# Kernel optimization log

Measured on AMD Instinct MI355X. Metric: run time of the kernel, lower is better.

## Reference

```python
import jax, jax.numpy as jnp
import numpy as np

N = 50000      # nodes
E = 800000     # edges (before self-loops)
H = 4          # heads
C = 64         # hidden channels per head
CLS = 10       # len(bins)+1
D_IN = 64      # input feature dim
NEG_SLOPE = 0.2


def setup_inputs() -> dict:
    key = jax.random.key(0)
    ks = jax.random.split(key, 24)
    inp = {
        "x": jax.random.normal(ks[0], (N, D_IN), jnp.float32),
        "edge_index": jax.random.randint(ks[1], (2, E), 0, N),
    }
    dims = [(D_IN, C), (H * C, C), (H * C, C), (H * C, C), (H * C, CLS)]
    k = 2
    for l, (din, dout) in enumerate(dims):
        sc = 1.0 / np.sqrt(din)
        inp[f"W{l}"] = jax.random.normal(ks[k], (din, H * dout), jnp.float32) * sc; k += 1
        inp[f"as{l}"] = jax.random.normal(ks[k], (H, dout), jnp.float32) * sc; k += 1
        inp[f"ad{l}"] = jax.random.normal(ks[k], (H, dout), jnp.float32) * sc; k += 1
        inp[f"b{l}"] = jnp.zeros((H * dout,), jnp.float32)
    return inp


def gat_layer(x, src, dst, W, a_s, a_d, b):
    # PyG GATConv (concat=True): h = x W -> [N,H,Ch]
    Hh, Ch = a_s.shape
    h = (x @ W).reshape(-1, Hh, Ch)
    asn = (h * a_s).sum(-1)                      # [N,H]
    adn = (h * a_d).sum(-1)                      # [N,H]
    e = jax.nn.leaky_relu(asn[src] + adn[dst], NEG_SLOPE)   # [Et,H]
    m = jax.ops.segment_max(e, dst, num_segments=N)         # softmax over in-edges per dst
    ex = jnp.exp(e - m[dst])
    s = jax.ops.segment_sum(ex, dst, num_segments=N)
    alpha = ex / (s[dst] + 1e-16)                # [Et,H]
    out = jax.ops.segment_sum(alpha[:, :, None] * h[src], dst, num_segments=N)
    return out.reshape(-1, Hh * Ch) + b


def reference(x, edge_index, W0, as0, ad0, b0, W1, as1, ad1, b1,
              W2, as2, ad2, b2, W3, as3, ad3, b3, W4, as4, ad4, b4):
    loop = jnp.arange(N, dtype=edge_index.dtype)  # GATConv add_self_loops=True
    src = jnp.concatenate([edge_index[0], loop])
    dst = jnp.concatenate([edge_index[1], loop])
    params = [(W0, as0, ad0, b0), (W1, as1, ad1, b1), (W2, as2, ad2, b2),
              (W3, as3, ad3, b3), (W4, as4, ad4, b4)]
    for W, a_s, a_d, b in params:
        x = jax.nn.relu(gat_layer(x, src, dst, W, a_s, a_d, b))
        # dropout(p=0.5) is identity in eval mode (training=False)
    return x
```

## Files before the change

kernel.cpp:

```cpp
#include <hip/hip_runtime.h>
#include <hip/hip_bf16.h>
#include <math.h>

#define N_NODES 50000
#define N_PAD   50048
#define N_EDGES 800000
#define HEADS 4

typedef __attribute__((ext_vector_type(8))) _Float16 half8_t;
typedef __attribute__((ext_vector_type(4))) _Float16 half4_t;
typedef __attribute__((ext_vector_type(4))) float f32x4;

__device__ inline void split2(float v, _Float16& p0, _Float16& p1) {
    p0 = (_Float16)v;
    p1 = (_Float16)(v - (float)p0);
}

__device__ inline size_t ktiled_off(int row, int k, size_t rowcap) {
    return (size_t)(k >> 5) * (rowcap * 32) + (size_t)row * 32 +
           ((((k >> 3) & 3) ^ (row & 3)) << 3) + (k & 7);
}


__global__ void init_deg_kernel(int* __restrict__ deg) {
    int i = blockIdx.x * blockDim.x + threadIdx.x;
    if (i < N_NODES) deg[i] = 1;
}

__global__ void hist_kernel(const int* __restrict__ dst, int* __restrict__ deg) {
    int i = blockIdx.x * blockDim.x + threadIdx.x;
    if (i < N_EDGES) atomicAdd(&deg[dst[i]], 1);
}

__global__ __launch_bounds__(1024) void scan_kernel(const int* __restrict__ deg,
                                                    int* __restrict__ rowptr,
                                                    int* __restrict__ cursor) {
    __shared__ int wsums[16];
    const int t = threadIdx.x;
    const int wv = t >> 6, ln = t & 63;
    const int WCHUNK = (N_NODES + 15) / 16;
    const int base = wv * WCHUNK;
    int lim = base + WCHUNK; if (lim > N_NODES) lim = N_NODES;

    int tot = 0;
    for (int i = base + ln; i < lim; i += 64) tot += deg[i];
#pragma unroll
    for (int o = 1; o < 64; o <<= 1) tot += __shfl_xor(tot, o);
    if (ln == 0) wsums[wv] = tot;
    __syncthreads();

    int run = 0;
    for (int w = 0; w < wv; ++w) run += wsums[w];

    for (int i0 = base; i0 < lim; i0 += 64) {
        int i = i0 + ln;
        int d = (i < lim) ? deg[i] : 0;
        int sc = d;
#pragma unroll
        for (int o = 1; o < 64; o <<= 1) {
            int v = __shfl_up(sc, o);
            if (ln >= o) sc += v;
        }
        if (i < lim) {
            int val = run + sc - d;
            rowptr[i] = val;
            cursor[i] = val;
        }
        run += __shfl(sc, 63);
    }
    if (t == 1023) rowptr[N_NODES] = run;
}

__global__ void scatter_kernel(const int* __restrict__ src, const int* __restrict__ dst,
                               int* __restrict__ cursor, int* __restrict__ col) {
    int i = blockIdx.x * blockDim.x + threadIdx.x;
    if (i < N_EDGES) {
        int d = dst[i];
        int pos = atomicAdd(&cursor[d], 1);
        col[pos] = src[i];
    } else if (i < N_EDGES + N_NODES) {
        int n = i - N_EDGES;
        int pos = atomicAdd(&cursor[n], 1);
        col[pos] = n;
    }
}


struct W5 { const float* p[5]; };

__global__ void w_split_kernel(W5 ws, _Float16* __restrict__ wt) {
    int t = blockIdx.x * blockDim.x + threadIdx.x;
    int l = t >> 16;
    int r = t & 65535;
    int c = r >> 8, k = r & 255;
    float v;
    if (l == 0) {
        v = ((k >> 6) == (c >> 6)) ? ws.p[0][(k & 63) * 256 + c] : 0.f;
    } else {
        int K = 256;
        int NC = (l == 4) ? 40 : 256;
        v = (k < K && c < NC) ? ws.p[l][k * NC + c] : 0.f;
    }
    _Float16 a, b;
    split2(v, a, b);
    size_t off = (size_t)l * 131072 + ktiled_off(c, k, 256);
    wt[off] = a;
    wt[65536 + off] = b;
}

__global__ void avec0_kernel(const float* __restrict__ W0,
                             const float* __restrict__ as0, const float* __restrict__ ad0,
                             float* __restrict__ avec, float* __restrict__ dvec) {
    int t = threadIdx.x;
    int hd = t >> 6, k = t & 63;
    float s1 = 0.f, s2 = 0.f;
    for (int c = 0; c < 64; ++c) {
        float w = W0[k * 256 + hd * 64 + c];
        s1 += w * as0[hd * 64 + c];
        s2 += w * ad0[hd * 64 + c];
    }
    avec[t] = s1;
    dvec[t] = s2;
}

__global__ void attn0_kernel(const float* __restrict__ x0,
                             const float* __restrict__ avec, const float* __restrict__ dvec,
                             float* __restrict__ asn, float* __restrict__ adn) {
    int t = blockIdx.x * blockDim.x + threadIdx.x;
    if (t >= N_NODES * HEADS) return;
    int n = t >> 2, hd = t & 3;
    const float* xp = x0 + (size_t)n * 64;
    const float* ap = avec + hd * 64;
    const float* dp = dvec + hd * 64;
    float s1 = 0.f, s2 = 0.f;
    for (int c = 0; c < 64; c += 4) {
        float4 xv = *reinterpret_cast<const float4*>(&xp[c]);
        float4 av = *reinterpret_cast<const float4*>(&ap[c]);
        float4 dv = *reinterpret_cast<const float4*>(&dp[c]);
        s1 += xv.x * av.x + xv.y * av.y + xv.z * av.z + xv.w * av.w;
        s2 += xv.x * dv.x + xv.y * dv.y + xv.z * dv.z + xv.w * dv.w;
    }
    asn[t] = s1;
    adn[t] = s2;
}


__global__ __launch_bounds__(256) void aggregate_x0_kernel(
        const float* __restrict__ x0,
        const float* __restrict__ asn, const float* __restrict__ adn,
        const int* __restrict__ rowptr, const int* __restrict__ col,
        _Float16* __restrict__ pl, size_t pstride) {
    const int n = (blockIdx.x << 2) + (threadIdx.x >> 6);
    const int lane = threadIdx.x & 63;
    const int hdg = lane >> 4;
    const int e16 = lane & 15;

    const int start = rowptr[n];
    const int end = rowptr[n + 1];
    const float adv = adn[(n << 2) | hdg];

    float m = -INFINITY, s = 0.f;
    float a0 = 0.f, a1 = 0.f, a2 = 0.f, a3 = 0.f;

    for (int e0 = start; e0 < end; e0 += 16) {
        int e = e0 + e16;
        int srcl = n;
        float ev = -INFINITY;
        if (e < end) {
            srcl = col[e];
            float t = asn[(srcl << 2) | hdg] + adv;
            ev = (t > 0.f) ? t : 0.2f * t;
        }
        float bm = ev;
#pragma unroll
        for (int o = 1; o < 16; o <<= 1) bm = fmaxf(bm, __shfl_xor(bm, o));
        float mn = fmaxf(m, bm);
        float scale = __expf(m - mn);
        float p = __expf(ev - mn);
        float ps = p;
#pragma unroll
        for (int o = 1; o < 16; o <<= 1) ps += __shfl_xor(ps, o);
        s = s * scale + ps;
        m = mn;

        a0 *= __shfl(scale, 0);
        a1 *= __shfl(scale, 16);
        a2 *= __shfl(scale, 32);
        a3 *= __shfl(scale, 48);

        int cnt = end - e0; if (cnt > 16) cnt = 16;
        int cnt4 = (cnt + 3) & ~3;
        for (int j0 = 0; j0 < cnt4; j0 += 4) {
#pragma unroll
            for (int j = 0; j < 4; ++j) {
                int sj = __shfl(srcl, j0 + j);
                float xv = x0[(size_t)sj * 64 + lane];
                a0 += __shfl(p, j0 + j) * xv;
                a1 += __shfl(p, 16 + j0 + j) * xv;
                a2 += __shfl(p, 32 + j0 + j) * xv;
                a3 += __shfl(p, 48 + j0 + j) * xv;
            }
        }
    }

    float v0 = a0 / (__shfl(s, 0) + 1e-16f);
    float v1 = a1 / (__shfl(s, 16) + 1e-16f);
    float v2 = a2 / (__shfl(s, 32) + 1e-16f);
    float v3 = a3 / (__shfl(s, 48) + 1e-16f);

    float vv[1];
    _Float16 pa, pb;
#define EMIT_Y0(V, HD)                                        \
    {                                                          \
        split2((V), pa, pb);                                   \
        size_t off = ktiled_off(n, (HD) * 64 + lane, N_PAD);   \
        pl[off] = pa;                                          \
        pl[pstride + off] = pb;                                \
    }
    EMIT_Y0(v0, 0) EMIT_Y0(v1, 1) EMIT_Y0(v2, 2) EMIT_Y0(v3, 3)
#undef EMIT_Y0
    (void)vv;
}


template <int FUSE_ATTN>
__global__ __launch_bounds__(256) void gemm_mfma_kernel(
        const _Float16* __restrict__ Apl, size_t apstride,
        const _Float16* __restrict__ Wt,
        float* __restrict__ C, int K, int NC,
        const float* __restrict__ as_flat, const float* __restrict__ ad_flat,
        float* __restrict__ asn, float* __restrict__ adn,
        const float* __restrict__ bias, _Float16* __restrict__ opl, size_t opstride) {
    __shared__ __align__(16) _Float16 lds[2][16384];

    const int tid = threadIdx.x;
    const int lane = tid & 63;
    const int wave = tid >> 6;
    const int wr = (wave >> 1) * 64;
    const int wc = (wave & 1) * 64;
    const int m0 = blockIdx.x * 128;
    const int n0 = blockIdx.y * 128;
    const bool wave_active = (FUSE_ATTN != 2) || ((n0 + wc) < NC);

    f32x4 acc[4][4];
#pragma unroll
    for (int i = 0; i < 4; ++i)
#pragma unroll
        for (int j = 0; j < 4; ++j) acc[i][j] = (f32x4){0.f, 0.f, 0.f, 0.f};

    const _Float16* gptr[8];
    size_t ktstep;
    {
        const _Float16* sbase;
        int rowbase;
        if (wave < 2) {
            sbase = Apl + (size_t)wave * apstride;
            rowbase = m0;
            ktstep = (size_t)N_PAD * 32;
        } else {
            sbase = Wt + (size_t)(wave - 2) * 65536;
            rowbase = n0;
            ktstep = 8192;
        }
#pragma unroll
        for (int it = 0; it < 8; ++it) {
            int idx = it * 64 + lane;
            gptr[it] = sbase + (size_t)(rowbase + (idx >> 2)) * 32 + (idx & 3) * 8;
        }
    }

    const int cswz = ((lane >> 4) ^ (lane & 3)) << 3;
    const int KT = K >> 5;

#pragma unroll
    for (int it = 0; it < 8; ++it) {
        __builtin_amdgcn_global_load_lds(
            (const __attribute__((address_space(1))) void*)gptr[it],
            (__attribute__((address_space(3))) void*)((char*)&lds[0][0] + wave * 8192 + it * 1024),
            16, 0, 0);
    }

    for (int kt = 0; kt < KT; ++kt) {
        __syncthreads();

        if (kt + 1 < KT) {
            char* dstw = (char*)&lds[(kt + 1) & 1][0] + wave * 8192;
#pragma unroll
            for (int it = 0; it < 8; ++it) {
                __builtin_amdgcn_global_load_lds(
                    (const __attribute__((address_space(1))) void*)(gptr[it] + (size_t)(kt + 1) * ktstep),
                    (__attribute__((address_space(3))) void*)(dstw + it * 1024),
                    16, 0, 0);
            }
        }

        if (wave_active) {
            const _Float16* Ab = &lds[kt & 1][0];
            const _Float16* Bb = Ab + 8192;

            half8_t bf[2][4];
#pragma unroll
            for (int p = 0; p < 2; ++p)
#pragma unroll
                for (int j = 0; j < 4; ++j) {
                    int r = wc + j * 16 + (lane & 15);
                    bf[p][j] = *(const half8_t*)(Bb + p * 4096 + r * 32 + cswz);
                }
#pragma unroll
            for (int i = 0; i < 4; ++i) {
                int r = wr + i * 16 + (lane & 15);
                half8_t af0 = *(const half8_t*)(Ab + r * 32 + cswz);
                half8_t af1 = *(const half8_t*)(Ab + 4096 + r * 32 + cswz);
#pragma unroll
                for (int j = 0; j < 4; ++j) {
                    f32x4 c = acc[i][j];
                    c = __builtin_amdgcn_mfma_f32_16x16x32_f16(af0, bf[1][j], c, 0, 0, 0);
                    c = __builtin_amdgcn_mfma_f32_16x16x32_f16(af1, bf[0][j], c, 0, 0, 0);
                    c = __builtin_amdgcn_mfma_f32_16x16x32_f16(af0, bf[0][j], c, 0, 0, 0);
                    acc[i][j] = c;
                }
            }
        }
    }

    const int rbase = m0 + wr + (lane >> 4) * 4;
    const int cbase = n0 + wc + (lane & 15);

    if (FUSE_ATTN == 1) {
#pragma unroll
        for (int i = 0; i < 4; ++i)
#pragma unroll
            for (int j = 0; j < 4; ++j) {
                int gcol = cbase + j * 16;
#pragma unroll
                for (int r4 = 0; r4 < 4; ++r4) {
                    int grow = rbase + i * 16 + r4;
                    if (grow < N_NODES) C[(size_t)grow * 256 + gcol] = acc[i][j][r4];
                }
            }
        const int hd_out = (n0 + wc) >> 6;
        float as_v[4], ad_v[4];
#pragma unroll
        for (int j = 0; j < 4; ++j) {
            int gc = cbase + j * 16;
            as_v[j] = as_flat[gc];
            ad_v[j] = ad_flat[gc];
        }
#pragma unroll
        for (int i = 0; i < 4; ++i)
#pragma unroll
            for (int r4 = 0; r4 < 4; ++r4) {
                float ps = 0.f, pd = 0.f;
#pragma unroll
                for (int j = 0; j < 4; ++j) {
                    float v = acc[i][j][r4];
                    ps += v * as_v[j];
                    pd += v * ad_v[j];
                }
#pragma unroll
                for (int o = 1; o < 16; o <<= 1) {
                    ps += __shfl_xor(ps, o);
                    pd += __shfl_xor(pd, o);
                }
                if ((lane & 15) == 0) {
                    int grow = rbase + i * 16 + r4;
                    if (grow < N_NODES) {
                        asn[grow * 4 + hd_out] = ps;
                        adn[grow * 4 + hd_out] = pd;
                    }
                }
            }
    } else if (FUSE_ATTN == 2) {
#pragma unroll
        for (int i = 0; i < 4; ++i)
#pragma unroll
            for (int j = 0; j < 4; ++j) {
                int gcol = cbase + j * 16;
                if (gcol >= NC) continue;
#pragma unroll
                for (int r4 = 0; r4 < 4; ++r4) {
                    int grow = rbase + i * 16 + r4;
                    if (grow < N_NODES) C[(size_t)grow * NC + gcol] = acc[i][j][r4];
                }
            }
        if (wc == 0) {
            float as_v[4], ad_v[4];
            int hdj[4];
#pragma unroll
            for (int j = 0; j < 4; ++j) {
                int gc = cbase + j * 16;
                bool valj = gc < 40;
                as_v[j] = valj ? as_flat[gc] : 0.f;
                ad_v[j] = valj ? ad_flat[gc] : 0.f;
                hdj[j] = valj ? (gc / 10) : -1;
            }
#pragma unroll
            for (int i = 0; i < 4; ++i)
#pragma unroll
                for (int r4 = 0; r4 < 4; ++r4) {
                    float p0 = 0.f, p1 = 0.f, p2 = 0.f, p3 = 0.f;
                    float q0 = 0.f, q1 = 0.f, q2 = 0.f, q3 = 0.f;
#pragma unroll
                    for (int j = 0; j < 4; ++j) {
                        float v = acc[i][j][r4];
                        float vs = v * as_v[j];
                        float vd = v * ad_v[j];
                        p0 += (hdj[j] == 0) ? vs : 0.f;
                        p1 += (hdj[j] == 1) ? vs : 0.f;
                        p2 += (hdj[j] == 2) ? vs : 0.f;
                        p3 += (hdj[j] == 3) ? vs : 0.f;
                        q0 += (hdj[j] == 0) ? vd : 0.f;
                        q1 += (hdj[j] == 1) ? vd : 0.f;
                        q2 += (hdj[j] == 2) ? vd : 0.f;
                        q3 += (hdj[j] == 3) ? vd : 0.f;
                    }
#pragma unroll
                    for (int o = 1; o < 16; o <<= 1) {
                        p0 += __shfl_xor(p0, o); p1 += __shfl_xor(p1, o);
                        p2 += __shfl_xor(p2, o); p3 += __shfl_xor(p3, o);
                        q0 += __shfl_xor(q0, o); q1 += __shfl_xor(q1, o);
                        q2 += __shfl_xor(q2, o); q3 += __shfl_xor(q3, o);
                    }
                    if ((lane & 15) == 0) {
                        int grow = rbase + i * 16 + r4;
                        if (grow < N_NODES) {
                            asn[grow * 4 + 0] = p0; asn[grow * 4 + 1] = p1;
                            asn[grow * 4 + 2] = p2; asn[grow * 4 + 3] = p3;
                            adn[grow * 4 + 0] = q0; adn[grow * 4 + 1] = q1;
                            adn[grow * 4 + 2] = q2; adn[grow * 4 + 3] = q3;
                        }
                    }
                }
        }
    } else {
#pragma unroll
        for (int i = 0; i < 4; ++i)
#pragma unroll
            for (int j = 0; j < 4; ++j) {
                int gcol = cbase + j * 16;
                float bv = bias[gcol];
#pragma unroll
                for (int r4 = 0; r4 < 4; ++r4) {
                    int grow = rbase + i * 16 + r4;
                    if (grow < N_NODES) {
                        float v = fmaxf(acc[i][j][r4] + bv, 0.f);
                        _Float16 pa, pb;
                        split2(v, pa, pb);
                        size_t off = ktiled_off(grow, gcol, N_PAD);
                        opl[off] = pa;
                        opl[opstride + off] = pb;
                    }
                }
            }
    }
}


__global__ __launch_bounds__(256) void aggregate64_kernel(
        const float* __restrict__ h,
        const float* __restrict__ asn, const float* __restrict__ adn,
        const int* __restrict__ rowptr, const int* __restrict__ col,
        const float* __restrict__ bias,
        _Float16* __restrict__ pl, size_t pstride) {
    const int n = (blockIdx.x << 2) + (threadIdx.x >> 6);
    const int lane = threadIdx.x & 63;
    const int hd = lane >> 4;
    const int e16 = lane & 15;
    const int pbase = lane & 48;

    const int start = rowptr[n];
    const int end = rowptr[n + 1];
    const float adv = adn[(n << 2) | hd];

    float m = -INFINITY, s = 0.f;
    float a0 = 0.f, a1 = 0.f, a2 = 0.f, a3 = 0.f;

    for (int e0 = start; e0 < end; e0 += 16) {
        int e = e0 + e16;
        int srcl = n;
        float ev = -INFINITY;
        if (e < end) {
            srcl = col[e];
            float t = asn[(srcl << 2) | hd] + adv;
            ev = (t > 0.f) ? t : 0.2f * t;
        }
        float bm = ev;
#pragma unroll
        for (int o = 1; o < 16; o <<= 1) bm = fmaxf(bm, __shfl_xor(bm, o));
        float mn = fmaxf(m, bm);
        float scale = __expf(m - mn);
        float p = __expf(ev - mn);
        float ps = p;
#pragma unroll
        for (int o = 1; o < 16; o <<= 1) ps += __shfl_xor(ps, o);
        s = s * scale + ps;
        a0 *= scale; a1 *= scale; a2 *= scale; a3 *= scale;
        m = mn;

        int cnt = end - e0; if (cnt > 16) cnt = 16;
        int cnt4 = (cnt + 3) & ~3;
        for (int j0 = 0; j0 < cnt4; j0 += 4) {
            int sj[4]; float pj[4];
#pragma unroll
            for (int j = 0; j < 4; ++j) {
                sj[j] = __shfl(srcl, j0 + j);
                pj[j] = __shfl(p, pbase + j0 + j);
            }
            float4 hv[4];
#pragma unroll
            for (int j = 0; j < 4; ++j)
                hv[j] = *reinterpret_cast<const float4*>(h + (size_t)sj[j] * 256 + (lane << 2));
#pragma unroll
            for (int j = 0; j < 4; ++j) {
                a0 += pj[j] * hv[j].x;
                a1 += pj[j] * hv[j].y;
                a2 += pj[j] * hv[j].z;
                a3 += pj[j] * hv[j].w;
            }
        }
    }

    float sd = s + 1e-16f;
    const float* bp = bias + (lane << 2);
    float v0 = fmaxf(a0 / sd + bp[0], 0.f);
    float v1 = fmaxf(a1 / sd + bp[1], 0.f);
    float v2 = fmaxf(a2 / sd + bp[2], 0.f);
    float v3 = fmaxf(a3 / sd + bp[3], 0.f);

    _Float16 s0a, s0b, s1a, s1b, s2a, s2b, s3a, s3b;
    split2(v0, s0a, s0b);
    split2(v1, s1a, s1b);
    split2(v2, s2a, s2b);
    split2(v3, s3a, s3b);
    half4_t o0, o1;
    o0[0] = s0a; o0[1] = s1a; o0[2] = s2a; o0[3] = s3a;
    o1[0] = s0b; o1[1] = s1b; o1[2] = s2b; o1[3] = s3b;

    const int kt = lane >> 3;
    const int cp = ((lane >> 1) & 3) ^ (n & 3);
    const int inner = (lane & 1) << 2;
    size_t off = (size_t)kt * ((size_t)N_PAD * 32) + (size_t)n * 32 + (cp << 3) + inner;
    *(half4_t*)(pl + off) = o0;
    *(half4_t*)(pl + pstride + off) = o1;
}


__global__ __launch_bounds__(256) void aggregate_out10_kernel(
        const float* __restrict__ h,
        const float* __restrict__ asn, const float* __restrict__ adn,
        const int* __restrict__ rowptr, const int* __restrict__ col,
        const float* __restrict__ bias, float* __restrict__ out) {
    const int n = (blockIdx.x << 2) + (threadIdx.x >> 6);
    const int lane = threadIdx.x & 63;
    const int hd16 = lane >> 4;
    const int e16 = lane & 15;
    const bool cvalid = lane < 40;
    const int hc = ((cvalid ? lane : 0) * 205) >> 11;

    const int start = rowptr[n];
    const int end = rowptr[n + 1];
    const float adv = adn[(n << 2) | hd16];

    float m = -INFINITY, s = 0.f, a0 = 0.f, a1 = 0.f;

    for (int e0 = start; e0 < end; e0 += 16) {
        int e = e0 + e16;
        int srcl = n;
        float ev = -INFINITY;
        if (e < end) {
            srcl = col[e];
            float t = asn[(srcl << 2) | hd16] + adv;
            ev = (t > 0.f) ? t : 0.2f * t;
        }
        float bm = ev;
#pragma unroll
        for (int o = 1; o < 16; o <<= 1) bm = fmaxf(bm, __shfl_xor(bm, o));
        float mn = fmaxf(m, bm);
        float scale = __expf(m - mn);
        float p = __expf(ev - mn);
        float ps = p;
#pragma unroll
        for (int o = 1; o < 16; o <<= 1) ps += __shfl_xor(ps, o);
        s = s * scale + ps;
        m = mn;

        float sc_c = __shfl(scale, hc * 16);
        a0 *= sc_c;
        a1 *= sc_c;

        int cnt = end - e0; if (cnt > 16) cnt = 16;
        int cnt4 = (cnt + 3) & ~3;
        for (int j0 = 0; j0 < cnt4; j0 += 4) {
            int sj[4]; float pj[4];
#pragma unroll
            for (int j = 0; j < 4; ++j) {
                sj[j] = __shfl(srcl, j0 + j);
                pj[j] = __shfl(p, hc * 16 + j0 + j);
            }
            float hv[4];
#pragma unroll
            for (int j = 0; j < 4; ++j)
                hv[j] = cvalid ? h[(size_t)sj[j] * 40 + lane] : 0.f;
            a0 += pj[0] * hv[0];
            a1 += pj[1] * hv[1];
            a0 += pj[2] * hv[2];
            a1 += pj[3] * hv[3];
        }
    }

    float sd = __shfl(s, hc * 16) + 1e-16f;
    if (cvalid) {
        float v = (a0 + a1) / sd + bias[lane];
        out[(size_t)n * 40 + lane] = fmaxf(v, 0.f);
    }
}


extern "C" void kernel_launch(void* const* d_in, const int* in_sizes, int n_in,
                              void* d_out, int out_size, void* d_ws, size_t ws_size,
                              hipStream_t stream) {
    const float* x_in = (const float*)d_in[0];
    const int* ei = (const int*)d_in[1];
    const int* src = ei;
    const int* dst = ei + N_EDGES;

    const float *AS[5], *AD[5], *BI[5];
    W5 w5;
    for (int l = 0; l < 5; ++l) {
        w5.p[l] = (const float*)d_in[2 + l * 4 + 0];
        AS[l] = (const float*)d_in[2 + l * 4 + 1];
        AD[l] = (const float*)d_in[2 + l * 4 + 2];
        BI[l] = (const float*)d_in[2 + l * 4 + 3];
    }

    const size_t PSTRIDE = (size_t)N_PAD * 256;
    _Float16* planes = (_Float16*)d_ws;
    float* hbuf = (float*)(planes + 2 * PSTRIDE);
    float* asn  = hbuf + (size_t)N_NODES * 256;
    float* adn  = asn + (size_t)N_NODES * HEADS;
    float* avec0 = adn + (size_t)N_NODES * HEADS;
    float* dvec0 = avec0 + 256;
    int* rowptr = (int*)(dvec0 + 256);
    int* cursor = rowptr + (N_NODES + 1);
    int* col    = cursor + N_NODES;
    _Float16* wt = (_Float16*)(((uintptr_t)(col + N_EDGES + N_NODES) + 15) & ~(uintptr_t)15);

    init_deg_kernel<<<(N_NODES + 255) / 256, 256, 0, stream>>>(cursor);
    hist_kernel<<<(N_EDGES + 255) / 256, 256, 0, stream>>>(dst, cursor);
    scan_kernel<<<1, 1024, 0, stream>>>(cursor, rowptr, cursor);
    scatter_kernel<<<(N_EDGES + N_NODES + 255) / 256, 256, 0, stream>>>(src, dst, cursor, col);

    w_split_kernel<<<5 * 65536 / 256, 256, 0, stream>>>(w5, wt);
    avec0_kernel<<<1, 256, 0, stream>>>(w5.p[0], AS[0], AD[0], avec0, dvec0);
    attn0_kernel<<<(N_NODES * HEADS + 255) / 256, 256, 0, stream>>>(
        x_in, avec0, dvec0, asn, adn);

    aggregate_x0_kernel<<<N_NODES / 4, 256, 0, stream>>>(
        x_in, asn, adn, rowptr, col, planes, PSTRIDE);
    {
        dim3 ggrid(N_PAD / 128, 2);
        gemm_mfma_kernel<3><<<ggrid, 256, 0, stream>>>(
            planes, PSTRIDE, wt, nullptr, 256, 256,
            nullptr, nullptr, nullptr, nullptr, BI[0], planes, PSTRIDE);
    }

    for (int l = 1; l < 5; ++l) {
        const int NC = (l == 4) ? 40 : 256;
        dim3 ggrid(N_PAD / 128, (NC + 127) / 128);
        const _Float16* wl = wt + (size_t)l * 131072;
        if (l < 4) {
            gemm_mfma_kernel<1><<<ggrid, 256, 0, stream>>>(
                planes, PSTRIDE, wl, hbuf, 256, NC, AS[l], AD[l], asn, adn,
                nullptr, nullptr, 0);
            aggregate64_kernel<<<N_NODES / 4, 256, 0, stream>>>(
                hbuf, asn, adn, rowptr, col, BI[l], planes, PSTRIDE);
        } else {
            gemm_mfma_kernel<2><<<ggrid, 256, 0, stream>>>(
                planes, PSTRIDE, wl, hbuf, 256, NC, AS[l], AD[l], asn, adn,
                nullptr, nullptr, 0);
            aggregate_out10_kernel<<<N_NODES / 4, 256, 0, stream>>>(
                hbuf, asn, adn, rowptr, col, BI[l], (float*)d_out);
        }
    }
    (void)in_sizes; (void)n_in; (void)out_size; (void)ws_size;
}
```

Baseline: 823.9 us.

## Load MFMA fragments directly from global into registers, dropping LDS staging

The GEMM kernel stops staging A and B tiles through double-buffered LDS with global_load_lds and block barriers. Instead each wave loads its own MFMA fragments straight from the pre-tiled, swizzled global layout into registers, prefetching the next k-tile while computing the current one. This removes the __syncthreads and the LDS round-trip, but B fragments are now loaded redundantly by the waves that share them, and the prefetch buffers raise register pressure.

```diff
diff --git a/kernel.cpp b/kernel.cpp
--- a/kernel.cpp
+++ b/kernel.cpp
@@ -208,7 +208,6 @@
     float v2 = a2 / (__shfl(s, 32) + 1e-16f);
     float v3 = a3 / (__shfl(s, 48) + 1e-16f);
 
-    float vv[1];
     _Float16 pa, pb;
 #define EMIT_Y0(V, HD)                                        \
     {                                                          \
@@ -219,7 +218,6 @@
     }
     EMIT_Y0(v0, 0) EMIT_Y0(v1, 1) EMIT_Y0(v2, 2) EMIT_Y0(v3, 3)
 #undef EMIT_Y0
-    (void)vv;
 }
 
 
@@ -231,8 +229,6 @@
         const float* __restrict__ as_flat, const float* __restrict__ ad_flat,
         float* __restrict__ asn, float* __restrict__ adn,
         const float* __restrict__ bias, _Float16* __restrict__ opl, size_t opstride) {
-    __shared__ __align__(16) _Float16 lds[2][16384];
-
     const int tid = threadIdx.x;
     const int lane = tid & 63;
     const int wave = tid >> 6;
@@ -248,78 +244,68 @@
 #pragma unroll
         for (int j = 0; j < 4; ++j) acc[i][j] = (f32x4){0.f, 0.f, 0.f, 0.f};
 
-    const _Float16* gptr[8];
-    size_t ktstep;
-    {
-        const _Float16* sbase;
-        int rowbase;
-        if (wave < 2) {
-            sbase = Apl + (size_t)wave * apstride;
-            rowbase = m0;
-            ktstep = (size_t)N_PAD * 32;
-        } else {
-            sbase = Wt + (size_t)(wave - 2) * 65536;
-            rowbase = n0;
-            ktstep = 8192;
-        }
-#pragma unroll
-        for (int it = 0; it < 8; ++it) {
-            int idx = it * 64 + lane;
-            gptr[it] = sbase + (size_t)(rowbase + (idx >> 2)) * 32 + (idx & 3) * 8;
-        }
-    }
-
     const int cswz = ((lane >> 4) ^ (lane & 3)) << 3;
+    const size_t aktstep = (size_t)N_PAD * 32;
+    const _Float16* abase = Apl + (size_t)(m0 + wr + (lane & 15)) * 32 + cswz;
+    const _Float16* bbase = Wt + (size_t)(n0 + wc + (lane & 15)) * 32 + cswz;
     const int KT = K >> 5;
 
-#pragma unroll
-    for (int it = 0; it < 8; ++it) {
-        __builtin_amdgcn_global_load_lds(
-            (const __attribute__((address_space(1))) void*)gptr[it],
-            (__attribute__((address_space(3))) void*)((char*)&lds[0][0] + wave * 8192 + it * 1024),
-            16, 0, 0);
+    half8_t afc[2][4], bfc[2][4];
+    if (wave_active) {
+#pragma unroll
+        for (int p = 0; p < 2; ++p)
+#pragma unroll
+            for (int i = 0; i < 4; ++i)
+                afc[p][i] = *(const half8_t*)(abase + p * apstride + i * 512);
+#pragma unroll
+        for (int p = 0; p < 2; ++p)
+#pragma unroll
+            for (int j = 0; j < 4; ++j)
+                bfc[p][j] = *(const half8_t*)(bbase + p * 65536 + j * 512);
     }
 
     for (int kt = 0; kt < KT; ++kt) {
-        __syncthreads();
-
-        if (kt + 1 < KT) {
-            char* dstw = (char*)&lds[(kt + 1) & 1][0] + wave * 8192;
-#pragma unroll
-            for (int it = 0; it < 8; ++it) {
-                __builtin_amdgcn_global_load_lds(
-                    (const __attribute__((address_space(1))) void*)(gptr[it] + (size_t)(kt + 1) * ktstep),
-                    (__attribute__((address_space(3))) void*)(dstw + it * 1024),
-                    16, 0, 0);
-            }
+        half8_t afn[2][4], bfn[2][4];
+        const bool more = (kt + 1 < KT);
+        if (wave_active && more) {
+            const size_t ao = (size_t)(kt + 1) * aktstep;
+            const size_t bo = (size_t)(kt + 1) * 8192;
+#pragma unroll
+            for (int p = 0; p < 2; ++p)
+#pragma unroll
+                for (int i = 0; i < 4; ++i)
+                    afn[p][i] = *(const half8_t*)(abase + p * apstride + ao + i * 512);
+#pragma unroll
+            for (int p = 0; p < 2; ++p)
+#pragma unroll
+                for (int j = 0; j < 4; ++j)
+                    bfn[p][j] = *(const half8_t*)(bbase + p * 65536 + bo + j * 512);
         }
 
         if (wave_active) {
-            const _Float16* Ab = &lds[kt & 1][0];
-            const _Float16* Bb = Ab + 8192;
-
-            half8_t bf[2][4];
-#pragma unroll
-            for (int p = 0; p < 2; ++p)
-#pragma unroll
-                for (int j = 0; j < 4; ++j) {
-                    int r = wc + j * 16 + (lane & 15);
-                    bf[p][j] = *(const half8_t*)(Bb + p * 4096 + r * 32 + cswz);
-                }
 #pragma unroll
             for (int i = 0; i < 4; ++i) {
-                int r = wr + i * 16 + (lane & 15);
-                half8_t af0 = *(const half8_t*)(Ab + r * 32 + cswz);
-                half8_t af1 = *(const half8_t*)(Ab + 4096 + r * 32 + cswz);
+                half8_t af0 = afc[0][i];
+                half8_t af1 = afc[1][i];
 #pragma unroll
                 for (int j = 0; j < 4; ++j) {
                     f32x4 c = acc[i][j];
-                    c = __builtin_amdgcn_mfma_f32_16x16x32_f16(af0, bf[1][j], c, 0, 0, 0);
-                    c = __builtin_amdgcn_mfma_f32_16x16x32_f16(af1, bf[0][j], c, 0, 0, 0);
-                    c = __builtin_amdgcn_mfma_f32_16x16x32_f16(af0, bf[0][j], c, 0, 0, 0);
+                    c = __builtin_amdgcn_mfma_f32_16x16x32_f16(af0, bfc[1][j], c, 0, 0, 0);
+                    c = __builtin_amdgcn_mfma_f32_16x16x32_f16(af1, bfc[0][j], c, 0, 0, 0);
+                    c = __builtin_amdgcn_mfma_f32_16x16x32_f16(af0, bfc[0][j], c, 0, 0, 0);
                     acc[i][j] = c;
                 }
             }
+        }
+
+        if (wave_active && more) {
+#pragma unroll
+            for (int p = 0; p < 2; ++p)
+#pragma unroll
+                for (int i = 0; i < 4; ++i) {
+                    afc[p][i] = afn[p][i];
+                    bfc[p][i] = bfn[p][i];
+                }
         }
     }
 
```

Result: slower. 846.2 us (+2.7%).
